# Performance work log

Measured on AMD Instinct MI355X. Metric: run time of the kernel, lower is better.

Reference implementation:

```python
import jax, jax.numpy as jnp
import numpy as np

V, E, S, B, N = 100000, 300, 1024, 64, 5
H = [512, 256, 128]

def setup_inputs() -> dict:
    key = jax.random.key(0)
    ks = jax.random.split(key, 10)
    x = jax.random.randint(ks[0], (B, S), 0, V, dtype=jnp.int32)
    # lengths must be >= n for valid n-gram counts (original assumes this)
    lengths = jax.random.randint(ks[1], (B,), N, S + 1, dtype=jnp.int32)
    sc = lambda f: 1.0 / np.sqrt(f)
    table = jax.random.normal(ks[2], (V, E), dtype=jnp.float32)
    W_slide = jax.random.uniform(ks[3], (N * E, H[0]), jnp.float32, -sc(N * E), sc(N * E))
    b_slide = jax.random.uniform(ks[4], (H[0],), jnp.float32, -sc(N * E), sc(N * E))
    W1 = jax.random.uniform(ks[5], (H[0], H[1]), jnp.float32, -sc(H[0]), sc(H[0]))
    b1 = jax.random.uniform(ks[6], (H[1],), jnp.float32, -sc(H[0]), sc(H[0]))
    W2 = jax.random.uniform(ks[7], (H[1], H[2]), jnp.float32, -sc(H[1]), sc(H[1]))
    b2 = jax.random.uniform(ks[8], (H[2],), jnp.float32, -sc(H[1]), sc(H[1]))
    return {"x": x, "lengths": lengths, "table": table, "W_slide": W_slide,
            "b_slide": b_slide, "W1": W1, "b1": b1, "W2": W2, "b2": b2}

def reference(x, lengths, table, W_slide, b_slide, W1, b1, W2, b2):
    n = N
    Wn = S - (n - 1)  # number of sliding windows per sequence
    emb = table[x]  # [B, S, E]
    # gather sliding windows: [B, Wn, n, E] -> [B, Wn, n*E]
    idx = jnp.arange(Wn)[:, None] + jnp.arange(n)[None, :]
    win = emb[:, idx].reshape(B, Wn, n * E)
    h = win @ W_slide + b_slide              # [B, Wn, H0]
    h = jax.nn.relu(h @ W1 + b1)             # [B, Wn, H1]
    h = jax.nn.relu(h @ W2 + b2)             # [B, Wn, H2]
    # ragged mean over valid n-gram positions per sample
    valid = (lengths - (n - 1)).astype(h.dtype)           # [B]
    mask = (jnp.arange(Wn)[None, :] < (lengths - (n - 1))[:, None]).astype(h.dtype)
    pooled = jnp.einsum('bwh,bw->bh', h, mask) / valid[:, None]
    return pooled
```

## Files before the change

### kernel.cpp

```cpp
#include <hip/hip_runtime.h>

#define B_N    64
#define S_LEN  1024
#define EMB    300
#define EMB_P  304
#define NGRAM  5
#define WPAD   1024
#define MTOT   (B_N * WPAD)
#define K1P    1536
#define H0     512
#define H1D    256
#define H2D    128
#define NK1    (K1P / 32)
#define NSTEP1 (K1P / 64)

#define GATHER_BLOCKS ((MTOT * 38) / 256)
#define WPREP_THREADS (H0 * K1P + H1D * H0 + H2D * H1D)
#define WPREP_BLOCKS  ((WPREP_THREADS + 255) / 256)

typedef _Float16 half8 __attribute__((ext_vector_type(8)));
typedef float  floatx4 __attribute__((ext_vector_type(4)));

typedef const __attribute__((address_space(1))) void* gptr_t;
typedef __attribute__((address_space(3))) void* sptr_t;

__device__ __forceinline__ void gload16(const void* g, void* s) {
  __builtin_amdgcn_global_load_lds((gptr_t)g, (sptr_t)s, 16, 0, 0);
}

__global__ void prep_kernel(const int* __restrict__ x,
                            const int* __restrict__ lengths,
                            const float* __restrict__ table,
                            _Float16* __restrict__ emb,
                            float* __restrict__ out,
                            const float* __restrict__ Ws,
                            const float* __restrict__ W1,
                            const float* __restrict__ W2,
                            _Float16* __restrict__ Bf1,
                            _Float16* __restrict__ Bf2,
                            _Float16* __restrict__ Bf3,
                            int* __restrict__ meta) {
  __shared__ int sN[64], sP[65], sN6[64], sP6[65];
  const int bid = blockIdx.x;
  if (bid < GATHER_BLOCKS) {
    if (bid < 32) out[bid * 256 + threadIdx.x] = 0.0f;
    int tid = bid * 256 + threadIdx.x;
    int tok = tid / 38;
    int c   = tid - tok * 38;
    int valid = lengths[tok >> 10] - (NGRAM - 1);
    int limit = ((valid + 127) & ~127) + (NGRAM - 1);
    if ((tok & 1023) >= limit) return;
    int e = c << 3;
    const float* row = table + (size_t)x[tok] * EMB + e;
    float4 v0 = *(const float4*)row;
    float4 v1 = make_float4(0.0f, 0.0f, 0.0f, 0.0f);
    if (e + 4 < EMB) v1 = *(const float4*)(row + 4);
    union { half8 h8; _Float16 h[8]; } u;
    u.h[0] = (_Float16)v0.x; u.h[1] = (_Float16)v0.y;
    u.h[2] = (_Float16)v0.z; u.h[3] = (_Float16)v0.w;
    u.h[4] = (_Float16)v1.x; u.h[5] = (_Float16)v1.y;
    u.h[6] = (_Float16)v1.z; u.h[7] = (_Float16)v1.w;
    *(half8*)(emb + (size_t)tok * EMB_P + e) = u.h8;
  } else if (bid < GATHER_BLOCKS + WPREP_BLOCKS) {
    int tid = (bid - GATHER_BLOCKS) * 256 + threadIdx.x;
    const int NS = H0 * K1P;
    const int N1 = H1D * H0;
    const int N2 = H2D * H1D;
    if (tid < NS) {
      int n = tid & 511, k = tid >> 9;
      float v = 0.0f;
      if (k < NGRAM * EMB_P) {
        int tn = k / EMB_P, e = k - tn * EMB_P;
        if (e < EMB) v = Ws[(size_t)(tn * EMB + e) * H0 + n];
      }
      int idx = ((((n >> 4) * NK1 + (k >> 5)) << 6) + (((k >> 3) & 3) << 4) + (n & 15)) * 8 + (k & 7);
      Bf1[idx] = (_Float16)v;
    } else if (tid < NS + N1) {
      int t = tid - NS;
      int n = t & 255, k = t >> 8;
      float v = W1[(size_t)k * H1D + n];
      int idx = ((((n >> 4) * 16 + (k >> 5)) << 6) + (((k >> 3) & 3) << 4) + (n & 15)) * 8 + (k & 7);
      Bf2[idx] = (_Float16)v;
    } else if (tid < NS + N1 + N2) {
      int t = tid - (NS + N1);
      int n = t & 127, k = t >> 7;
      float v = W2[(size_t)k * H2D + n];
      int idx = ((((n >> 4) * 8 + (k >> 5)) << 6) + (((k >> 3) & 3) << 4) + (n & 15)) * 8 + (k & 7);
      Bf3[idx] = (_Float16)v;
    }
  } else {
    int t = threadIdx.x;
    if (t < 64) {
      int valid = lengths[t] - (NGRAM - 1);
      sN[t]  = (valid + 127) >> 7;
      sN6[t] = (valid + 63) >> 6;
    }
    __syncthreads();
    if (t == 0) {
      int s = 0, s6 = 0;
      for (int i = 0; i < 64; i++) {
        sP[i] = s;   s  += sN[i];
        sP6[i] = s6; s6 += sN6[i];
      }
      meta[0] = s; meta[1] = s6;
    }
    __syncthreads();
    if (t < 64) {
      int base = sP[t], n = sN[t];
      for (int i = 0; i < n; i++) meta[8 + base + i] = (t << 3) + i;
      int b6 = sP6[t], n6 = sN6[t];
      for (int i = 0; i < n6; i++) meta[520 + b6 + i] = (t << 4) + i;
    }
  }
}

__global__ __launch_bounds__(256, 3)
void gemm1(const _Float16* __restrict__ A, const _Float16* __restrict__ Bf,
           const float* __restrict__ bias, _Float16* __restrict__ Cf,
           const int* __restrict__ meta) {
  __shared__ _Float16 sm[16384];

  const int nLive4 = meta[0] << 2;
  const int xcd = blockIdx.x & 7, bi = blockIdx.x >> 3;
  const int q = nLive4 >> 3, r = nLive4 & 7;
  if (bi >= q + (xcd < r ? 1 : 0)) return;
  const int L = xcd * q + (xcd < r ? xcd : r) + bi;
  const int mt = meta[8 + (L >> 2)], nt = L & 3;

  const int tid  = threadIdx.x;
  const int wave = tid >> 6, lane = tid & 63;
  const int wr   = wave >> 1, wc = wave & 1;
  const int quad = lane >> 4, l16 = lane & 15;

  const long mBase = (long)mt << 7;
  const int  nBase = nt << 7;

  const int srow0  = (wave << 3) + (lane >> 3);
  const int schunk = lane & 7;
  const _Float16* aG[4];
  int sOffA[4];
#pragma unroll
  for (int p = 0; p < 4; p++) {
    int row = (p << 5) + srow0;
    int c   = schunk ^ (row & 7);
    aG[p]   = A + (mBase + row) * EMB_P + (c << 3);
    sOffA[p] = (row << 6) + (schunk << 3);
  }

  const _Float16* bSrc[4];
  int sOffB[4];
#pragma unroll
  for (int p = 0; p < 4; p++) {
    int idx    = (p << 8) + tid;
    int n16l   = idx >> 7;
    int s      = (idx >> 6) & 1;
    int lane_s = idx & 63;
    bSrc[p]  = Bf + (((size_t)((nBase >> 4) + n16l) * NK1 + s) << 9) + (lane_s << 3);
    sOffB[p] = 8192 + (idx << 3);
  }

  int aOff[2][4];
#pragma unroll
  for (int s = 0; s < 2; s++)
#pragma unroll
    for (int i = 0; i < 4; i++) {
      int rr   = (wr << 6) + (i << 4) + l16;
      int slot = ((s << 2) + quad) ^ (l16 & 7);
      aOff[s][i] = (rr << 6) + (slot << 3);
    }
  int bOff[2][4];
#pragma unroll
  for (int s = 0; s < 2; s++)
#pragma unroll
    for (int j = 0; j < 4; j++)
      bOff[s][j] = 8192 + ((((((wc << 2) + j) << 1) + s) << 9) + (lane << 3));

  floatx4 acc[4][4] = {};

#pragma unroll 2
  for (int kk = 0; kk < NSTEP1; kk++) {
    __syncthreads();
    const int koA = kk << 6;
    const size_t koB = (size_t)kk << 10;
#pragma unroll
    for (int p = 0; p < 4; p++) gload16(aG[p] + koA, &sm[sOffA[p]]);
#pragma unroll
    for (int p = 0; p < 4; p++) gload16(bSrc[p] + koB, &sm[sOffB[p]]);
    __syncthreads();
#pragma unroll
    for (int s = 0; s < 2; s++) {
      half8 aFr[4], bFr[4];
#pragma unroll
      for (int i = 0; i < 4; i++)
        aFr[i] = *(const half8*)(&sm[aOff[s][i]]);
#pragma unroll
      for (int j = 0; j < 4; j++)
        bFr[j] = *(const half8*)(&sm[bOff[s][j]]);
#pragma unroll
      for (int i = 0; i < 4; i++)
#pragma unroll
        for (int j = 0; j < 4; j++)
          acc[i][j] = __builtin_amdgcn_mfma_f32_16x16x32_f16(aFr[i], bFr[j], acc[i][j], 0, 0, 0);
    }
  }

  __syncthreads();
  _Float16* cs = &sm[0];
#pragma unroll
  for (int j = 0; j < 4; j++) {
    int cl = (wc << 6) + (j << 4) + l16;
    float bv = bias[nBase + cl];
    int ksl = cl >> 5;
    int sub_hi = ((cl >> 3) & 3) << 4;
    int c7 = cl & 7;
#pragma unroll
    for (int i = 0; i < 4; i++) {
      int m16l = (wr << 2) + i;
#pragma unroll
      for (int rr = 0; rr < 4; rr++) {
        int ml = (quad << 2) + rr;
        cs[(((m16l << 2) + ksl) << 9) + ((sub_hi + ml) << 3) + c7] =
            (_Float16)(acc[i][j][rr] + bv);
      }
    }
  }
  __syncthreads();
#pragma unroll
  for (int it = 0; it < 8; it++) {
    int cid = (it << 2) + wave;
    int m16l = cid >> 2, ksl = cid & 3;
    size_t g = ((size_t)(((mt << 3) + m16l) * 16 + (nt << 2) + ksl) << 9) + (lane << 3);
    *(half8*)(Cf + g) = *(const half8*)(cs + (cid << 9) + (lane << 3));
  }
}

__global__ __launch_bounds__(256, 3)
void gemm23(const _Float16* __restrict__ Af, const _Float16* __restrict__ B2,
            const _Float16* __restrict__ B3, const float* __restrict__ bias1,
            const float* __restrict__ bias2, float* __restrict__ out,
            const int* __restrict__ lengths, const int* __restrict__ meta) {
  __shared__ _Float16 sH[16384];

  if ((int)blockIdx.x >= meta[1]) return;
  const int mt = meta[520 + blockIdx.x];

  const int tid  = threadIdx.x;
  const int wave = tid >> 6, lane = tid & 63;
  const int wc   = wave;
  const int quad = lane >> 4, l16 = lane & 15;

  const int b = mt >> 4;
  const int validw = lengths[b] - (NGRAM - 1);

  const _Float16* aB = Af + (((size_t)(mt << 2) * 16) << 9) + (lane << 3);
  const _Float16* bB = B2 + ((size_t)wc << 15) + (lane << 3);

  floatx4 acc2[4][4] = {};
  half8 aP[4], bP[4], aQ[4], bQ[4];

  auto loadA = [&](half8* d, int kk) {
#pragma unroll
    for (int i = 0; i < 4; i++)
      d[i] = *(const half8*)(aB + ((size_t)kk << 9) + ((size_t)i << 13));
  };
  auto loadB = [&](half8* d, int kk) {
#pragma unroll
    for (int j = 0; j < 4; j++)
      d[j] = *(const half8*)(bB + ((size_t)kk << 9) + ((size_t)j << 13));
  };
  auto mfmaStep = [&](const half8* aF, const half8* bF) {
    __builtin_amdgcn_s_setprio(1);
#pragma unroll
    for (int i = 0; i < 4; i++)
#pragma unroll
      for (int j = 0; j < 4; j++)
        acc2[i][j] = __builtin_amdgcn_mfma_f32_16x16x32_f16(aF[i], bF[j], acc2[i][j], 0, 0, 0);
    __builtin_amdgcn_s_setprio(0);
  };

  loadA(aP, 0); loadB(bP, 0);
#pragma unroll
  for (int kk = 0; kk < 16; kk += 2) {
    loadA(aQ, kk + 1); loadB(bQ, kk + 1);
    mfmaStep(aP, bP);
    if (kk + 2 < 16) { loadA(aP, kk + 2); loadB(bP, kk + 2); }
    mfmaStep(aQ, bQ);
  }

#pragma unroll
  for (int j = 0; j < 4; j++) {
    int n = (wc << 6) + (j << 4) + l16;
    float bv = bias1[n];
    int ks = n >> 5;
    int sub_hi = ((n >> 3) & 3) << 4;
    int c7 = n & 7;
#pragma unroll
    for (int i = 0; i < 4; i++) {
#pragma unroll
      for (int rr = 0; rr < 4; rr++) {
        int ml = (quad << 2) + rr;
        sH[(((i << 3) + ks) << 9) + ((sub_hi + ml) << 3) + c7] =
            (_Float16)fmaxf(acc2[i][j][rr] + bv, 0.0f);
      }
    }
  }
  __syncthreads();

  const _Float16* b3R[2];
#pragma unroll
  for (int j = 0; j < 2; j++)
    b3R[j] = B3 + (((size_t)((wc << 1) + j) * 8) << 9) + (lane << 3);

  floatx4 acc3[4][2] = {};
#pragma unroll
  for (int ks = 0; ks < 8; ks++) {
    half8 aF[4], bF[2];
#pragma unroll
    for (int i = 0; i < 4; i++)
      aF[i] = *(const half8*)(sH + (((i << 3) + ks) << 9) + (lane << 3));
#pragma unroll
    for (int j = 0; j < 2; j++) bF[j] = *(const half8*)(b3R[j] + ((size_t)ks << 9));
    __builtin_amdgcn_s_setprio(1);
#pragma unroll
    for (int i = 0; i < 4; i++)
#pragma unroll
      for (int j = 0; j < 2; j++)
        acc3[i][j] = __builtin_amdgcn_mfma_f32_16x16x32_f16(aF[i], bF[j], acc3[i][j], 0, 0, 0);
    __builtin_amdgcn_s_setprio(0);
  }

  float inv = 1.0f / (float)validw;
  int wBase = (mt & 15) << 6;
#pragma unroll
  for (int j = 0; j < 2; j++) {
    int col = (wc << 5) + (j << 4) + l16;
    float bv = bias2[col];
    float p = 0.0f;
#pragma unroll
    for (int i = 0; i < 4; i++) {
#pragma unroll
      for (int rr = 0; rr < 4; rr++) {
        int w = wBase + (i << 4) + (quad << 2) + rr;
        float v = fmaxf(acc3[i][j][rr] + bv, 0.0f);
        p += (w < validw) ? v : 0.0f;
      }
    }
    p *= inv;
    p += __shfl_xor(p, 16, 64);
    p += __shfl_xor(p, 32, 64);
    if (quad == 0) atomicAdd(out + b * H2D + col, p);
  }
}

extern "C" void kernel_launch(void* const* d_in, const int* in_sizes, int n_in,
                              void* d_out, int out_size, void* d_ws, size_t ws_size,
                              hipStream_t stream) {
  const int*   x       = (const int*)d_in[0];
  const int*   lengths = (const int*)d_in[1];
  const float* table   = (const float*)d_in[2];
  const float* W_slide = (const float*)d_in[3];
  const float* b_slide = (const float*)d_in[4];
  const float* W1      = (const float*)d_in[5];
  const float* b1      = (const float*)d_in[6];
  const float* W2      = (const float*)d_in[7];
  const float* b2      = (const float*)d_in[8];
  float* out = (float*)d_out;

  _Float16* ws  = (_Float16*)d_ws;
  _Float16* emb = ws;
  _Float16* Bf1 = emb + (size_t)MTOT * EMB_P + 4096;
  _Float16* Bf2 = Bf1 + (size_t)H0 * K1P;
  _Float16* Bf3 = Bf2 + (size_t)H1D * H0;
  _Float16* h1f = Bf3 + (size_t)H2D * H1D;
  int*      meta = (int*)(h1f + (size_t)MTOT * H0);

  prep_kernel<<<GATHER_BLOCKS + WPREP_BLOCKS + 1, 256, 0, stream>>>(
      x, lengths, table, emb, out, W_slide, W1, W2, Bf1, Bf2, Bf3, meta);
  gemm1<<<(MTOT / 128) * (H0 / 128), 256, 0, stream>>>(emb, Bf1, b_slide, h1f, meta);
  gemm23<<<MTOT / 64, 256, 0, stream>>>(h1f, Bf2, Bf3, b1, b2, out, lengths, meta);
}
```

Measured before the change: 264.2 us.

## Fuse gemm23 into gemm1 via last-arriving-block counter per M tile

Removes the separate gemm23 launch. Each gemm1 block increments a per-M-tile counter after writing its N slice. The block that completes the fourth slice then runs the layer-2/3 MLP and pooling for both 64-row halves of that tile. Per-tile counters are zeroed in the prep kernel, and the 64-row tile list in meta is dropped. This aims to cut a kernel launch and the tail between kernels and to overlap the MLP with gemm1 tiles still running, at the cost of an atomic, threadfences, and uneven extra work on the last-arriving blocks.

```diff
diff --git a/kernel.cpp b/kernel.cpp
--- a/kernel.cpp
+++ b/kernel.cpp
@@ -40,7 +40,7 @@
                             _Float16* __restrict__ Bf2,
                             _Float16* __restrict__ Bf3,
                             int* __restrict__ meta) {
-  __shared__ int sN[64], sP[65], sN6[64], sP6[65];
+  __shared__ int sN[64], sP[65];
   const int bid = blockIdx.x;
   if (bid < GATHER_BLOCKS) {
     if (bid < 32) out[bid * 256 + threadIdx.x] = 0.0f;
@@ -90,35 +90,149 @@
     }
   } else {
     int t = threadIdx.x;
+    meta[1536 + t] = 0;
+    meta[1536 + 256 + t] = 0;
     if (t < 64) {
       int valid = lengths[t] - (NGRAM - 1);
-      sN[t]  = (valid + 127) >> 7;
-      sN6[t] = (valid + 63) >> 6;
+      sN[t] = (valid + 127) >> 7;
     }
     __syncthreads();
     if (t == 0) {
-      int s = 0, s6 = 0;
-      for (int i = 0; i < 64; i++) {
-        sP[i] = s;   s  += sN[i];
-        sP6[i] = s6; s6 += sN6[i];
-      }
-      meta[0] = s; meta[1] = s6;
+      int s = 0;
+      for (int i = 0; i < 64; i++) { sP[i] = s; s += sN[i]; }
+      meta[0] = s;
     }
     __syncthreads();
     if (t < 64) {
       int base = sP[t], n = sN[t];
       for (int i = 0; i < n; i++) meta[8 + base + i] = (t << 3) + i;
-      int b6 = sP6[t], n6 = sN6[t];
-      for (int i = 0; i < n6; i++) meta[520 + b6 + i] = (t << 4) + i;
-    }
+    }
+  }
+}
+
+__device__ void gemm23_tile(_Float16* sm,
+                            const _Float16* __restrict__ Af,
+                            const _Float16* __restrict__ B2,
+                            const _Float16* __restrict__ B3,
+                            const float* __restrict__ bias1,
+                            const float* __restrict__ bias2,
+                            float* __restrict__ out,
+                            int validw, int mt64) {
+  const int tid  = threadIdx.x;
+  const int wave = tid >> 6, lane = tid & 63;
+  const int wc   = wave;
+  const int quad = lane >> 4, l16 = lane & 15;
+  const int b = mt64 >> 4;
+
+  const _Float16* aB = Af + (((size_t)(mt64 << 2) * 16) << 9) + (lane << 3);
+  const _Float16* bB = B2 + ((size_t)wc << 15) + (lane << 3);
+
+  floatx4 acc2[4][4] = {};
+  half8 aP[4], bP[4], aQ[4], bQ[4];
+
+  auto loadA = [&](half8* d, int kk) {
+#pragma unroll
+    for (int i = 0; i < 4; i++)
+      d[i] = *(const half8*)(aB + ((size_t)kk << 9) + ((size_t)i << 13));
+  };
+  auto loadB = [&](half8* d, int kk) {
+#pragma unroll
+    for (int j = 0; j < 4; j++)
+      d[j] = *(const half8*)(bB + ((size_t)kk << 9) + ((size_t)j << 13));
+  };
+  auto mfmaStep = [&](const half8* aF, const half8* bF) {
+    __builtin_amdgcn_s_setprio(1);
+#pragma unroll
+    for (int i = 0; i < 4; i++)
+#pragma unroll
+      for (int j = 0; j < 4; j++)
+        acc2[i][j] = __builtin_amdgcn_mfma_f32_16x16x32_f16(aF[i], bF[j], acc2[i][j], 0, 0, 0);
+    __builtin_amdgcn_s_setprio(0);
+  };
+
+  loadA(aP, 0); loadB(bP, 0);
+#pragma unroll
+  for (int kk = 0; kk < 16; kk += 2) {
+    loadA(aQ, kk + 1); loadB(bQ, kk + 1);
+    mfmaStep(aP, bP);
+    if (kk + 2 < 16) { loadA(aP, kk + 2); loadB(bP, kk + 2); }
+    mfmaStep(aQ, bQ);
+  }
+
+#pragma unroll
+  for (int j = 0; j < 4; j++) {
+    int n = (wc << 6) + (j << 4) + l16;
+    float bv = bias1[n];
+    int ks = n >> 5;
+    int sub_hi = ((n >> 3) & 3) << 4;
+    int c7 = n & 7;
+#pragma unroll
+    for (int i = 0; i < 4; i++) {
+#pragma unroll
+      for (int rr = 0; rr < 4; rr++) {
+        int ml = (quad << 2) + rr;
+        sm[(((i << 3) + ks) << 9) + ((sub_hi + ml) << 3) + c7] =
+            (_Float16)fmaxf(acc2[i][j][rr] + bv, 0.0f);
+      }
+    }
+  }
+  __syncthreads();
+
+  const _Float16* b3R[2];
+#pragma unroll
+  for (int j = 0; j < 2; j++)
+    b3R[j] = B3 + (((size_t)((wc << 1) + j) * 8) << 9) + (lane << 3);
+
+  floatx4 acc3[4][2] = {};
+#pragma unroll
+  for (int ks = 0; ks < 8; ks++) {
+    half8 aF[4], bF[2];
+#pragma unroll
+    for (int i = 0; i < 4; i++)
+      aF[i] = *(const half8*)(sm + (((i << 3) + ks) << 9) + (lane << 3));
+#pragma unroll
+    for (int j = 0; j < 2; j++) bF[j] = *(const half8*)(b3R[j] + ((size_t)ks << 9));
+    __builtin_amdgcn_s_setprio(1);
+#pragma unroll
+    for (int i = 0; i < 4; i++)
+#pragma unroll
+      for (int j = 0; j < 2; j++)
+        acc3[i][j] = __builtin_amdgcn_mfma_f32_16x16x32_f16(aF[i], bF[j], acc3[i][j], 0, 0, 0);
+    __builtin_amdgcn_s_setprio(0);
+  }
+
+  float inv = 1.0f / (float)validw;
+  int wBase = (mt64 & 15) << 6;
+#pragma unroll
+  for (int j = 0; j < 2; j++) {
+    int col = (wc << 5) + (j << 4) + l16;
+    float bv = bias2[col];
+    float p = 0.0f;
+#pragma unroll
+    for (int i = 0; i < 4; i++) {
+#pragma unroll
+      for (int rr = 0; rr < 4; rr++) {
+        int w = wBase + (i << 4) + (quad << 2) + rr;
+        float v = fmaxf(acc3[i][j][rr] + bv, 0.0f);
+        p += (w < validw) ? v : 0.0f;
+      }
+    }
+    p *= inv;
+    p += __shfl_xor(p, 16, 64);
+    p += __shfl_xor(p, 32, 64);
+    if (quad == 0) atomicAdd(out + b * H2D + col, p);
   }
 }
 
 __global__ __launch_bounds__(256, 3)
 void gemm1(const _Float16* __restrict__ A, const _Float16* __restrict__ Bf,
            const float* __restrict__ bias, _Float16* __restrict__ Cf,
-           const int* __restrict__ meta) {
+           const int* __restrict__ meta, int* __restrict__ cnt,
+           const _Float16* __restrict__ B2, const _Float16* __restrict__ B3,
+           const float* __restrict__ b1v, const float* __restrict__ b2v,
+           float* __restrict__ out, const int* __restrict__ lengths) {
   __shared__ _Float16 sm[16384];
+  __shared__ int sLast;
 
   const int nLive4 = meta[0] << 2;
   const int xcd = blockIdx.x & 7, bi = blockIdx.x >> 3;
@@ -232,123 +346,17 @@
     size_t g = ((size_t)(((mt << 3) + m16l) * 16 + (nt << 2) + ksl) << 9) + (lane << 3);
     *(half8*)(Cf + g) = *(const half8*)(cs + (cid << 9) + (lane << 3));
   }
-}
-
-__global__ __launch_bounds__(256, 3)
-void gemm23(const _Float16* __restrict__ Af, const _Float16* __restrict__ B2,
-            const _Float16* __restrict__ B3, const float* __restrict__ bias1,
-            const float* __restrict__ bias2, float* __restrict__ out,
-            const int* __restrict__ lengths, const int* __restrict__ meta) {
-  __shared__ _Float16 sH[16384];
-
-  if ((int)blockIdx.x >= meta[1]) return;
-  const int mt = meta[520 + blockIdx.x];
-
-  const int tid  = threadIdx.x;
-  const int wave = tid >> 6, lane = tid & 63;
-  const int wc   = wave;
-  const int quad = lane >> 4, l16 = lane & 15;
-
-  const int b = mt >> 4;
-  const int validw = lengths[b] - (NGRAM - 1);
-
-  const _Float16* aB = Af + (((size_t)(mt << 2) * 16) << 9) + (lane << 3);
-  const _Float16* bB = B2 + ((size_t)wc << 15) + (lane << 3);
-
-  floatx4 acc2[4][4] = {};
-  half8 aP[4], bP[4], aQ[4], bQ[4];
-
-  auto loadA = [&](half8* d, int kk) {
-#pragma unroll
-    for (int i = 0; i < 4; i++)
-      d[i] = *(const half8*)(aB + ((size_t)kk << 9) + ((size_t)i << 13));
-  };
-  auto loadB = [&](half8* d, int kk) {
-#pragma unroll
-    for (int j = 0; j < 4; j++)
-      d[j] = *(const half8*)(bB + ((size_t)kk << 9) + ((size_t)j << 13));
-  };
-  auto mfmaStep = [&](const half8* aF, const half8* bF) {
-    __builtin_amdgcn_s_setprio(1);
-#pragma unroll
-    for (int i = 0; i < 4; i++)
-#pragma unroll
-      for (int j = 0; j < 4; j++)
-        acc2[i][j] = __builtin_amdgcn_mfma_f32_16x16x32_f16(aF[i], bF[j], acc2[i][j], 0, 0, 0);
-    __builtin_amdgcn_s_setprio(0);
-  };
-
-  loadA(aP, 0); loadB(bP, 0);
-#pragma unroll
-  for (int kk = 0; kk < 16; kk += 2) {
-    loadA(aQ, kk + 1); loadB(bQ, kk + 1);
-    mfmaStep(aP, bP);
-    if (kk + 2 < 16) { loadA(aP, kk + 2); loadB(bP, kk + 2); }
-    mfmaStep(aQ, bQ);
-  }
-
-#pragma unroll
-  for (int j = 0; j < 4; j++) {
-    int n = (wc << 6) + (j << 4) + l16;
-    float bv = bias1[n];
-    int ks = n >> 5;
-    int sub_hi = ((n >> 3) & 3) << 4;
-    int c7 = n & 7;
-#pragma unroll
-    for (int i = 0; i < 4; i++) {
-#pragma unroll
-      for (int rr = 0; rr < 4; rr++) {
-        int ml = (quad << 2) + rr;
-        sH[(((i << 3) + ks) << 9) + ((sub_hi + ml) << 3) + c7] =
-            (_Float16)fmaxf(acc2[i][j][rr] + bv, 0.0f);
-      }
-    }
-  }
-  __syncthreads();
-
-  const _Float16* b3R[2];
-#pragma unroll
-  for (int j = 0; j < 2; j++)
-    b3R[j] = B3 + (((size_t)((wc << 1) + j) * 8) << 9) + (lane << 3);
-
-  floatx4 acc3[4][2] = {};
-#pragma unroll
-  for (int ks = 0; ks < 8; ks++) {
-    half8 aF[4], bF[2];
-#pragma unroll
-    for (int i = 0; i < 4; i++)
-      aF[i] = *(const half8*)(sH + (((i << 3) + ks) << 9) + (lane << 3));
-#pragma unroll
-    for (int j = 0; j < 2; j++) bF[j] = *(const half8*)(b3R[j] + ((size_t)ks << 9));
-    __builtin_amdgcn_s_setprio(1);
-#pragma unroll
-    for (int i = 0; i < 4; i++)
-#pragma unroll
-      for (int j = 0; j < 2; j++)
-        acc3[i][j] = __builtin_amdgcn_mfma_f32_16x16x32_f16(aF[i], bF[j], acc3[i][j], 0, 0, 0);
-    __builtin_amdgcn_s_setprio(0);
-  }
-
-  float inv = 1.0f / (float)validw;
-  int wBase = (mt & 15) << 6;
-#pragma unroll
-  for (int j = 0; j < 2; j++) {
-    int col = (wc << 5) + (j << 4) + l16;
-    float bv = bias2[col];
-    float p = 0.0f;
-#pragma unroll
-    for (int i = 0; i < 4; i++) {
-#pragma unroll
-      for (int rr = 0; rr < 4; rr++) {
-        int w = wBase + (i << 4) + (quad << 2) + rr;
-        float v = fmaxf(acc3[i][j][rr] + bv, 0.0f);
-        p += (w < validw) ? v : 0.0f;
-      }
-    }
-    p *= inv;
-    p += __shfl_xor(p, 16, 64);
-    p += __shfl_xor(p, 32, 64);
-    if (quad == 0) atomicAdd(out + b * H2D + col, p);
+
+  __threadfence();
+  __syncthreads();
+  if (tid == 0) sLast = (atomicAdd(&cnt[mt], 1) == 3) ? 1 : 0;
+  __syncthreads();
+  if (sLast) {
+    __threadfence();
+    const int validw = lengths[mt >> 3] - (NGRAM - 1);
+    gemm23_tile(sm, Cf, B2, B3, b1v, b2v, out, validw, mt << 1);
+    __syncthreads();
+    gemm23_tile(sm, Cf, B2, B3, b1v, b2v, out, validw, (mt << 1) + 1);
   }
 }
 
@@ -376,6 +384,7 @@
 
   prep_kernel<<<GATHER_BLOCKS + WPREP_BLOCKS + 1, 256, 0, stream>>>(
       x, lengths, table, emb, out, W_slide, W1, W2, Bf1, Bf2, Bf3, meta);
-  gemm1<<<(MTOT / 128) * (H0 / 128), 256, 0, stream>>>(emb, Bf1, b_slide, h1f, meta);
-  gemm23<<<MTOT / 64, 256, 0, stream>>>(h1f, Bf2, Bf3, b1, b2, out, lengths, meta);
-}
+  gemm1<<<(MTOT / 128) * (H0 / 128), 256, 0, stream>>>(
+      emb, Bf1, b_slide, h1f, meta, meta + 1536,
+      Bf2, Bf3, b1, b2, out, lengths);
+}
```

New measurement: 470.3 us. +78.1%, slower.
